# Optimization experiments

Hardware: AMD Instinct MI355X
Metric: run time of the kernel (lower is better)

## Reference

```python
import jax, jax.numpy as jnp
import numpy as np

B, T, C, H = 8, 2048, 1024, 64  # batch, seq_len(block_size), embedding_size, head_size


def setup_inputs() -> dict:
    key = jax.random.key(0)
    kx, kk, kq, kv = jax.random.split(key, 4)
    x = jax.random.normal(kx, (B, T, C), dtype=jnp.float32)
    # nn.Linear(C, H, bias=False) weights, stored as [in, out] for x @ W
    s = 1.0 / np.sqrt(C)
    Wk = jax.random.uniform(kk, (C, H), dtype=jnp.float32, minval=-s, maxval=s)
    Wq = jax.random.uniform(kq, (C, H), dtype=jnp.float32, minval=-s, maxval=s)
    Wv = jax.random.uniform(kv, (C, H), dtype=jnp.float32, minval=-s, maxval=s)
    return {"x": x, "Wk": Wk, "Wq": Wq, "Wv": Wv}


def reference(x, Wk, Wq, Wv):
    Bx, Tx, Cx = x.shape
    k = jnp.einsum('btc,ch->bth', x, Wk)
    q = jnp.einsum('btc,ch->bth', x, Wq)
    v = jnp.einsum('btc,ch->bth', x, Wv)
    # NOTE: original scales by embedding dim C ** -0.5, not head_size
    scores = jnp.einsum('bth,bsh->bts', q, k) * (Cx ** -0.5)  # [B,T,T]
    causal = jnp.tril(jnp.ones((Tx, Tx), dtype=bool))
    scores = jnp.where(causal, scores, -jnp.inf)
    attn = jax.nn.softmax(scores, axis=-1)
    # dropout is identity in eval/deterministic mode
    out = jnp.einsum('bts,bsh->bth', attn, v)  # [B,T,H]
    return out
```

## Files before the change

### kernel.cpp

```cpp
#include <hip/hip_runtime.h>
#include <hip/hip_bf16.h>
#include <math.h>


#define BT 16384
#define TSEQ 2048
#define XST 72

typedef __attribute__((ext_vector_type(8))) __bf16 bf16x8;
typedef __attribute__((ext_vector_type(8))) unsigned short ushort8;
typedef __attribute__((ext_vector_type(4))) float floatx4;

#define MFMA16(a, b, c) __builtin_amdgcn_mfma_f32_16x16x32_bf16( \
    __builtin_bit_cast(bf16x8, (a)), __builtin_bit_cast(bf16x8, (b)), (c), 0, 0, 0)

__device__ inline unsigned short f2bf(float f) {
  unsigned u = __builtin_bit_cast(unsigned, f);
  u += 0x7FFFu + ((u >> 16) & 1u);
  return (unsigned short)(u >> 16);
}
__device__ inline float bf2f(unsigned short s) {
  return __builtin_bit_cast(float, (unsigned)s << 16);
}
__device__ inline unsigned long long pack4bf(floatx4 f) {
  return (unsigned long long)f2bf(f[0]) | ((unsigned long long)f2bf(f[1]) << 16) |
         ((unsigned long long)f2bf(f[2]) << 32) | ((unsigned long long)f2bf(f[3]) << 48);
}
__device__ inline ushort8 pack8bf(floatx4 a, floatx4 b) {
  ushort8 t;
#pragma unroll
  for (int i = 0; i < 4; ++i) t[i] = f2bf(a[i]);
#pragma unroll
  for (int i = 0; i < 4; ++i) t[4 + i] = f2bf(b[i]);
  return t;
}
__device__ inline void glds16(const unsigned short* g, unsigned short* l) {
  __builtin_amdgcn_global_load_lds(
      (const __attribute__((address_space(1))) unsigned int*)g,
      (__attribute__((address_space(3))) unsigned int*)l, 16, 0, 0);
}

__global__ __launch_bounds__(256) void wt2_kernel(
    const float* __restrict__ Wq, const float* __restrict__ Wk,
    const float* __restrict__ Wv, unsigned short* __restrict__ Wt2) {
  __shared__ float ls[64][65];
  const int m = blockIdx.x >> 4;
  const int kci = blockIdx.x & 15;
  const int c0 = kci << 6;
  const float* __restrict__ W = (m == 0) ? Wq : (m == 1) ? Wk : Wv;
  const int tid = threadIdx.x;
#pragma unroll
  for (int i = 0; i < 16; ++i) {
    int idx = tid + (i << 8);
    int cl = idx >> 6, h = idx & 63;
    ls[cl][h] = W[(c0 + cl) * 64 + h];
  }
  __syncthreads();
  const int w = tid >> 6, lane = tid & 63;
  const int quad = lane >> 4, l16 = lane & 15;
  const int nt = (m << 2) + w;
#pragma unroll
  for (int half = 0; half < 2; ++half) {
    ushort8 t;
#pragma unroll
    for (int j = 0; j < 8; ++j)
      t[j] = f2bf(ls[(half << 5) + (quad << 3) + j][(w << 4) + l16]);
    *(ushort8*)(Wt2 + ((size_t)(((nt << 4) + kci) * 2 + half) << 9) +
                (lane << 3)) = t;
  }
}

#define BB0 9216
#define BBS 12288
#define XBS 4608

__global__ __launch_bounds__(512) void qkv_mfma(
    const float* __restrict__ x, const unsigned short* __restrict__ Wt2,
    unsigned short* __restrict__ Qf, unsigned short* __restrict__ Kf,
    unsigned short* __restrict__ Vf) {
  __shared__ unsigned short smem[33792];

  const int tid = threadIdx.x;
  const int w = tid >> 6, lane = tid & 63;
  const int quad = lane >> 4, l16 = lane & 15;
  const int wr = w >> 2, wn = w & 3;
  const int r0 = blockIdx.x << 6;

  const int xrow = (w << 3) + (lane >> 3);
  const int xcol = (lane & 7) << 3;
  const float* __restrict__ xp = x + (size_t)(r0 + xrow) * 1024 + xcol;
  const int xw_u16 = xrow * XST + xcol;

  floatx4 acc[2][3];
#pragma unroll
  for (int rt = 0; rt < 2; ++rt)
#pragma unroll
    for (int n = 0; n < 3; ++n) acc[rt][n] = (floatx4){0.f, 0.f, 0.f, 0.f};

  floatx4 pf[2][2];

#pragma unroll
  for (int i = 0; i < 3; ++i) {
    const int f = 3 * w + i;
    glds16(Wt2 + ((size_t)(((f >> 1) << 4) * 2 + (f & 1)) << 9) + (lane << 3),
           &smem[BB0 + (f << 9)]);
  }
  pf[0][0] = *(const floatx4*)(xp);
  pf[0][1] = *(const floatx4*)(xp + 4);
  pf[1][0] = *(const floatx4*)(xp + 64);
  pf[1][1] = *(const floatx4*)(xp + 68);
  *(ushort8*)&smem[xw_u16] = pack8bf(pf[0][0], pf[0][1]);
  asm volatile("s_waitcnt lgkmcnt(0)");
  __builtin_amdgcn_sched_barrier(0);
  __builtin_amdgcn_s_barrier();
  __builtin_amdgcn_sched_barrier(0);

#pragma unroll
  for (int c = 0; c < 16; ++c) {
    const int cur = c & 1, nxt = cur ^ 1;
    if (c + 1 < 16) {
#pragma unroll
      for (int i = 0; i < 3; ++i) {
        const int f = 3 * w + i;
        glds16(Wt2 + ((size_t)((((f >> 1) << 4) + (c + 1)) * 2 + (f & 1)) << 9) +
                   (lane << 3),
               &smem[BB0 + nxt * BBS + (f << 9)]);
      }
      *(ushort8*)&smem[nxt * XBS + xw_u16] =
          pack8bf(pf[(c + 1) & 1][0], pf[(c + 1) & 1][1]);
    }
    if (c + 2 < 16) {
      pf[c & 1][0] = *(const floatx4*)(xp + ((c + 2) << 6));
      pf[c & 1][1] = *(const floatx4*)(xp + ((c + 2) << 6) + 4);
    }
    __builtin_amdgcn_sched_barrier(0);

    ushort8 af[2][2];
#pragma unroll
    for (int rt = 0; rt < 2; ++rt)
#pragma unroll
      for (int h = 0; h < 2; ++h)
        af[rt][h] = *(const ushort8*)&smem[cur * XBS +
            ((wr << 5) + (rt << 4) + l16) * XST + (h << 5) + (quad << 3)];
    ushort8 bfr[3][2];
#pragma unroll
    for (int n = 0; n < 3; ++n)
#pragma unroll
      for (int h = 0; h < 2; ++h)
        bfr[n][h] = *(const ushort8*)&smem[BB0 + cur * BBS +
            ((((3 * wn + n) << 1) + h) << 9) + (lane << 3)];
#pragma unroll
    for (int h = 0; h < 2; ++h)
#pragma unroll
      for (int rt = 0; rt < 2; ++rt)
#pragma unroll
        for (int n = 0; n < 3; ++n)
          acc[rt][n] = MFMA16(af[rt][h], bfr[n][h], acc[rt][n]);

    __builtin_amdgcn_sched_barrier(0);
    if (c < 14) { asm volatile("s_waitcnt vmcnt(2)"); }
    else        { asm volatile("s_waitcnt vmcnt(0)"); }
    asm volatile("s_waitcnt lgkmcnt(0)");
    __builtin_amdgcn_sched_barrier(0);
    __builtin_amdgcn_s_barrier();
    __builtin_amdgcn_sched_barrier(0);
  }

#pragma unroll
  for (int n = 0; n < 3; ++n) {
    const int nt = 3 * wn + n;
    const int m = nt >> 2, hg = nt & 3;
#pragma unroll
    for (int rt = 0; rt < 2; ++rt) {
      const int rowb = (wr << 5) + (rt << 4) + (quad << 2);
      if (m < 2) {
#pragma unroll
        for (int r = 0; r < 4; ++r)
          smem[m * XBS + (rowb + r) * XST + (hg << 4) + l16] =
              f2bf(acc[rt][n][r]);
      } else {
        *(unsigned long long*)&smem[2 * XBS + ((hg << 4) + l16) * XST + rowb] =
            pack4bf(acc[rt][n]);
      }
    }
  }
  __syncthreads();

  const int b = blockIdx.x >> 5, st = blockIdx.x & 31;
#pragma unroll
  for (int i = 0; i < 3; ++i) {
    const int f = w * 3 + i;
    const int m = f >> 3, idx = f & 7, grp = idx >> 1, kh = idx & 1;
    ushort8 t = *(const ushort8*)&smem[m * XBS + ((grp << 4) + l16) * XST +
                                       (kh << 5) + (quad << 3)];
    unsigned short* dst;
    if (m == 0)
      dst = Qf + (((size_t)(b * 128 + (st << 2) + grp) * 2 + kh) << 9);
    else if (m == 1)
      dst = Kf + (((size_t)((b * 32 + st) * 4 + grp) * 2 + kh) << 9);
    else
      dst = Vf + (((size_t)((b * 32 + st) * 4 + grp) * 2 + kh) << 9);
    *(ushort8*)(dst + (lane << 3)) = t;
  }
}

__global__ __launch_bounds__(128) void attn_part(
    const unsigned short* __restrict__ Qf, const unsigned short* __restrict__ Kf,
    const unsigned short* __restrict__ Vf, float* __restrict__ part) {
  __shared__ unsigned short Pw[2][16 * XST];

  const int tid = threadIdx.x;
  const int w = tid >> 6, lane = tid & 63;
  const int quad = lane >> 4, l16 = lane & 15;
  const int b = blockIdx.x / 288;
  const int rem = blockIdx.x - b * 288;
  const int e = rem >> 1, half = rem & 1;
  int g = 0;
#pragma unroll
  for (int gg = 1; gg < 8; ++gg) g += (e >= 2 * gg * (gg + 1)) ? 1 : 0;
  const int rem2 = e - 2 * g * (g + 1);
  const int qt = (g << 2) + rem2 / (g + 1);
  const int ch = rem2 - (rem2 / (g + 1)) * (g + 1);
  const int s0 = ch << 2;
  const int s1 = min(s0 + 4, qt + 1);
  const int rg = (half << 1) + w;
  const int r16 = (qt << 2) + rg;

  const unsigned short* qbase =
      Qf + ((((size_t)b * 128 + r16) * 2) << 9) + (lane << 3);
  ushort8 qf0 = *(const ushort8*)qbase;
  ushort8 qf1 = *(const ushort8*)(qbase + 512);

  floatx4 acc[4], lacc;
#pragma unroll
  for (int nt = 0; nt < 4; ++nt) acc[nt] = (floatx4){0.f, 0.f, 0.f, 0.f};
  lacc = (floatx4){0.f, 0.f, 0.f, 0.f};
  const ushort8 ones = {0x3F80, 0x3F80, 0x3F80, 0x3F80,
                        0x3F80, 0x3F80, 0x3F80, 0x3F80};

#define KVIDX(ss, nt, kh) \
  (((((size_t)(b * 32 + (ss)) << 2) + (nt)) * 2 + (kh)) << 9)

  ushort8 bk[4][2];
#pragma unroll
  for (int nt = 0; nt < 4; ++nt)
#pragma unroll
    for (int kh = 0; kh < 2; ++kh)
      bk[nt][kh] = *(const ushort8*)(Kf + KVIDX(s0, nt, kh) + (lane << 3));

  for (int s = s0; s < s1; ++s) {
    const int sn = (s + 1 < s1) ? s + 1 : s;
    ushort8 bv[4][2];
#pragma unroll
    for (int nt = 0; nt < 4; ++nt)
#pragma unroll
      for (int kh = 0; kh < 2; ++kh)
        bv[nt][kh] = *(const ushort8*)(Vf + KVIDX(s, nt, kh) + (lane << 3));
    ushort8 bkn[4][2];
#pragma unroll
    for (int nt = 0; nt < 4; ++nt)
#pragma unroll
      for (int kh = 0; kh < 2; ++kh)
        bkn[nt][kh] = *(const ushort8*)(Kf + KVIDX(sn, nt, kh) + (lane << 3));

    floatx4 sf[4];
#pragma unroll
    for (int nt = 0; nt < 4; ++nt) {
      sf[nt] = (floatx4){0.f, 0.f, 0.f, 0.f};
      sf[nt] = MFMA16(qf0, bk[nt][0], sf[nt]);
      sf[nt] = MFMA16(qf1, bk[nt][1], sf[nt]);
    }

    const bool diag = (s == qt);
    const int qrow = (rg << 4) + (quad << 2);
#pragma unroll
    for (int nt = 0; nt < 4; ++nt) {
      const int keyl = (nt << 4) + l16;
#pragma unroll
      for (int r = 0; r < 4; ++r) {
        float ev = __expf(sf[nt][r] * 0.03125f);
        if (diag && keyl > ((qt << 6) - (qt << 6)) + qrow + r) ev = 0.f;
        Pw[w][((quad << 2) + r) * XST + keyl] = f2bf(ev);
      }
    }

#pragma unroll
    for (int kh = 0; kh < 2; ++kh) {
      ushort8 pa = *(const ushort8*)&Pw[w][l16 * XST + (kh << 5) + (quad << 3)];
      lacc = MFMA16(pa, ones, lacc);
#pragma unroll
      for (int nt = 0; nt < 4; ++nt) acc[nt] = MFMA16(pa, bv[nt][kh], acc[nt]);
    }
#pragma unroll
    for (int nt = 0; nt < 4; ++nt) {
      bk[nt][0] = bkn[nt][0];
      bk[nt][1] = bkn[nt][1];
    }
  }
#undef KVIDX

  float* slot = part + (size_t)(b * 144 + e) * 2112;
  if (l16 == 0) {
#pragma unroll
    for (int r = 0; r < 4; ++r) slot[(rg << 4) + (quad << 2) + r] = lacc[r];
  }
  unsigned short* op = (unsigned short*)(slot + 64);
#pragma unroll
  for (int nt = 0; nt < 4; ++nt)
#pragma unroll
    for (int r = 0; r < 4; ++r)
      op[((rg << 4) + (quad << 2) + r) * 64 + (nt << 4) + l16] = f2bf(acc[nt][r]);
}

__global__ __launch_bounds__(256) void attn_combine(
    const float* __restrict__ part, float* __restrict__ out) {
  const int rh = blockIdx.x & 1;
  const int bqt = blockIdx.x >> 1;
  const int b = bqt >> 5, qt = bqt & 31;
  const int tid = threadIdx.x;
  const int row = (rh << 5) + (tid >> 3);
  const int hseg = (tid & 7) << 3;
  const int g = qt >> 2;
  const int nch = g + 1;
  const int ebase = 2 * g * (g + 1) + (qt & 3) * (g + 1);

  float l = 0.f;
  float ov[8];
#pragma unroll
  for (int i = 0; i < 8; ++i) ov[i] = 0.f;
  for (int c = 0; c < nch; ++c) {
    const float* slot = part + (size_t)(b * 144 + ebase + c) * 2112;
    l += slot[row];
    ushort8 o0 = *(const ushort8*)((const unsigned short*)(slot + 64) +
                                   row * 64 + hseg);
#pragma unroll
    for (int i = 0; i < 8; ++i) ov[i] += bf2f(o0[i]);
  }
  const float inv = 1.f / l;
  float* o = out + ((size_t)(b * TSEQ + (qt << 6) + row)) * 64 + hseg;
#pragma unroll
  for (int i = 0; i < 8; ++i) o[i] = ov[i] * inv;
}

extern "C" void kernel_launch(void* const* d_in, const int* in_sizes, int n_in,
                              void* d_out, int out_size, void* d_ws, size_t ws_size,
                              hipStream_t stream) {
  const float* x  = (const float*)d_in[0];
  const float* Wk = (const float*)d_in[1];
  const float* Wq = (const float*)d_in[2];
  const float* Wv = (const float*)d_in[3];

  unsigned short* Qfw = (unsigned short*)d_ws;
  unsigned short* Kfw = Qfw + (size_t)BT * 64;
  unsigned short* Vfw = Kfw + (size_t)BT * 64;
  unsigned short* Wt2 = Vfw + (size_t)BT * 64;
  float* part = (float*)(Wt2 + 3 * 64 * 1024);

  wt2_kernel<<<48, 256, 0, stream>>>(Wq, Wk, Wv, Wt2);
  qkv_mfma<<<256, 512, 0, stream>>>(x, Wt2, Qfw, Kfw, Vfw);
  attn_part<<<2304, 128, 0, stream>>>(Qfw, Kfw, Vfw, part);
  attn_combine<<<512, 256, 0, stream>>>(part, (float*)d_out);
}
```

Measured before the change: 132.5 us.

## Fuse all four stages into one cooperative persistent kernel with grid syncs

Replaces the four separate launches (weight transpose, QKV projection, partial attention, combine) with a single cooperative kernel of 256 blocks that separates the phases with grid.sync. The attention phase becomes a persistent loop in which each wave handles work units. The QKV GEMM weight pipeline also moves from double to triple buffering with a deeper prefetch. The aim is to remove launch gaps and kernel boundaries, at the cost of grid-wide barriers and less parallelism in the attention phase (256 blocks instead of 2304).

```diff
diff --git a/kernel.cpp b/kernel.cpp
--- a/kernel.cpp
+++ b/kernel.cpp
@@ -1,6 +1,9 @@
 #include <hip/hip_runtime.h>
 #include <hip/hip_bf16.h>
+#include <hip/hip_cooperative_groups.h>
 #include <math.h>
+
+namespace cg = cooperative_groups;
 
 
 #define BT 16384
@@ -40,306 +43,320 @@
       (__attribute__((address_space(3))) unsigned int*)l, 16, 0, 0);
 }
 
-__global__ __launch_bounds__(256) void wt2_kernel(
-    const float* __restrict__ Wq, const float* __restrict__ Wk,
-    const float* __restrict__ Wv, unsigned short* __restrict__ Wt2) {
-  __shared__ float ls[64][65];
-  const int m = blockIdx.x >> 4;
-  const int kci = blockIdx.x & 15;
-  const int c0 = kci << 6;
-  const float* __restrict__ W = (m == 0) ? Wq : (m == 1) ? Wk : Wv;
-  const int tid = threadIdx.x;
-#pragma unroll
-  for (int i = 0; i < 16; ++i) {
-    int idx = tid + (i << 8);
-    int cl = idx >> 6, h = idx & 63;
-    ls[cl][h] = W[(c0 + cl) * 64 + h];
-  }
-  __syncthreads();
-  const int w = tid >> 6, lane = tid & 63;
-  const int quad = lane >> 4, l16 = lane & 15;
-  const int nt = (m << 2) + w;
-#pragma unroll
-  for (int half = 0; half < 2; ++half) {
-    ushort8 t;
-#pragma unroll
-    for (int j = 0; j < 8; ++j)
-      t[j] = f2bf(ls[(half << 5) + (quad << 3) + j][(w << 4) + l16]);
-    *(ushort8*)(Wt2 + ((size_t)(((nt << 4) + kci) * 2 + half) << 9) +
-                (lane << 3)) = t;
-  }
-}
-
+#define XBS 4608
 #define BB0 9216
 #define BBS 12288
-#define XBS 4608
-
-__global__ __launch_bounds__(512) void qkv_mfma(
-    const float* __restrict__ x, const unsigned short* __restrict__ Wt2,
-    unsigned short* __restrict__ Qf, unsigned short* __restrict__ Kf,
-    unsigned short* __restrict__ Vf) {
-  __shared__ unsigned short smem[33792];
-
+
+__global__ __launch_bounds__(512, 2) void fused_attn(
+    const float* __restrict__ x, const float* __restrict__ Wq,
+    const float* __restrict__ Wk, const float* __restrict__ Wv,
+    unsigned short* __restrict__ Wt2, unsigned short* __restrict__ Qf,
+    unsigned short* __restrict__ Kf, unsigned short* __restrict__ Vf,
+    float* __restrict__ part, float* __restrict__ out) {
+  __shared__ __align__(16) unsigned short smem[46080];
   const int tid = threadIdx.x;
   const int w = tid >> 6, lane = tid & 63;
   const int quad = lane >> 4, l16 = lane & 15;
-  const int wr = w >> 2, wn = w & 3;
-  const int r0 = blockIdx.x << 6;
-
-  const int xrow = (w << 3) + (lane >> 3);
-  const int xcol = (lane & 7) << 3;
-  const float* __restrict__ xp = x + (size_t)(r0 + xrow) * 1024 + xcol;
-  const int xw_u16 = xrow * XST + xcol;
-
-  floatx4 acc[2][3];
-#pragma unroll
-  for (int rt = 0; rt < 2; ++rt)
-#pragma unroll
-    for (int n = 0; n < 3; ++n) acc[rt][n] = (floatx4){0.f, 0.f, 0.f, 0.f};
-
-  floatx4 pf[2][2];
-
-#pragma unroll
-  for (int i = 0; i < 3; ++i) {
-    const int f = 3 * w + i;
-    glds16(Wt2 + ((size_t)(((f >> 1) << 4) * 2 + (f & 1)) << 9) + (lane << 3),
-           &smem[BB0 + (f << 9)]);
+  cg::grid_group grid = cg::this_grid();
+
+  if (blockIdx.x < 48) {
+    float* ls = (float*)smem;
+    const int m = blockIdx.x >> 4, kci = blockIdx.x & 15, c0 = kci << 6;
+    const float* __restrict__ W = (m == 0) ? Wq : (m == 1) ? Wk : Wv;
+#pragma unroll
+    for (int i = 0; i < 8; ++i) {
+      int idx = tid + (i << 9);
+      int cl = idx >> 6, h = idx & 63;
+      ls[cl * 65 + h] = W[(c0 + cl) * 64 + h];
+    }
+    __syncthreads();
+    if (tid < 256) {
+      const int nt = (m << 2) + w;
+#pragma unroll
+      for (int half = 0; half < 2; ++half) {
+        ushort8 t;
+#pragma unroll
+        for (int j = 0; j < 8; ++j)
+          t[j] = f2bf(ls[((half << 5) + (quad << 3) + j) * 65 + (w << 4) + l16]);
+        *(ushort8*)(Wt2 + ((size_t)(((nt << 4) + kci) * 2 + half) << 9) +
+                    (lane << 3)) = t;
+      }
+    }
   }
-  pf[0][0] = *(const floatx4*)(xp);
-  pf[0][1] = *(const floatx4*)(xp + 4);
-  pf[1][0] = *(const floatx4*)(xp + 64);
-  pf[1][1] = *(const floatx4*)(xp + 68);
-  *(ushort8*)&smem[xw_u16] = pack8bf(pf[0][0], pf[0][1]);
-  asm volatile("s_waitcnt lgkmcnt(0)");
-  __builtin_amdgcn_sched_barrier(0);
-  __builtin_amdgcn_s_barrier();
-  __builtin_amdgcn_sched_barrier(0);
-
-#pragma unroll
-  for (int c = 0; c < 16; ++c) {
-    const int cur = c & 1, nxt = cur ^ 1;
-    if (c + 1 < 16) {
-#pragma unroll
-      for (int i = 0; i < 3; ++i) {
-        const int f = 3 * w + i;
-        glds16(Wt2 + ((size_t)((((f >> 1) << 4) + (c + 1)) * 2 + (f & 1)) << 9) +
-                   (lane << 3),
-               &smem[BB0 + nxt * BBS + (f << 9)]);
-      }
-      *(ushort8*)&smem[nxt * XBS + xw_u16] =
-          pack8bf(pf[(c + 1) & 1][0], pf[(c + 1) & 1][1]);
-    }
-    if (c + 2 < 16) {
-      pf[c & 1][0] = *(const floatx4*)(xp + ((c + 2) << 6));
-      pf[c & 1][1] = *(const floatx4*)(xp + ((c + 2) << 6) + 4);
-    }
-    __builtin_amdgcn_sched_barrier(0);
-
-    ushort8 af[2][2];
+  __threadfence();
+  grid.sync();
+
+  {
+    const int wr = w >> 2, wn = w & 3;
+    const int r0 = blockIdx.x << 6;
+    const int xrow = (w << 3) + (lane >> 3);
+    const int xcol = (lane & 7) << 3;
+    const float* __restrict__ xp = x + (size_t)(r0 + xrow) * 1024 + xcol;
+    const int xw_u16 = xrow * XST + xcol;
+
+    floatx4 acc[2][3];
 #pragma unroll
     for (int rt = 0; rt < 2; ++rt)
 #pragma unroll
+      for (int n = 0; n < 3; ++n) acc[rt][n] = (floatx4){0.f, 0.f, 0.f, 0.f};
+
+    floatx4 pf[2][2];
+    pf[0][0] = *(const floatx4*)(xp);
+    pf[0][1] = *(const floatx4*)(xp + 4);
+    __builtin_amdgcn_sched_barrier(0);
+#pragma unroll
+    for (int i = 0; i < 3; ++i) {
+      const int f = 3 * w + i;
+      glds16(Wt2 + ((size_t)(((f >> 1) << 4) * 2 + (f & 1)) << 9) + (lane << 3),
+             &smem[BB0 + (f << 9)]);
+    }
+    __builtin_amdgcn_sched_barrier(0);
+    pf[1][0] = *(const floatx4*)(xp + 64);
+    pf[1][1] = *(const floatx4*)(xp + 68);
+    __builtin_amdgcn_sched_barrier(0);
+#pragma unroll
+    for (int i = 0; i < 3; ++i) {
+      const int f = 3 * w + i;
+      glds16(Wt2 + ((size_t)((((f >> 1) << 4) + 1) * 2 + (f & 1)) << 9) +
+                 (lane << 3),
+             &smem[BB0 + BBS + (f << 9)]);
+    }
+    __builtin_amdgcn_sched_barrier(0);
+    *(ushort8*)&smem[xw_u16] = pack8bf(pf[0][0], pf[0][1]);
+    __builtin_amdgcn_sched_barrier(0);
+    asm volatile("s_waitcnt vmcnt(5)");
+    asm volatile("s_waitcnt lgkmcnt(0)");
+    __builtin_amdgcn_sched_barrier(0);
+    __builtin_amdgcn_s_barrier();
+    __builtin_amdgcn_sched_barrier(0);
+
+#pragma unroll
+    for (int c = 0; c < 16; ++c) {
+      if (c + 1 < 16)
+        *(ushort8*)&smem[((c + 1) & 1) * XBS + xw_u16] =
+            pack8bf(pf[(c + 1) & 1][0], pf[(c + 1) & 1][1]);
+      __builtin_amdgcn_sched_barrier(0);
+      if (c + 2 < 16) {
+        pf[c & 1][0] = *(const floatx4*)(xp + ((c + 2) << 6));
+        pf[c & 1][1] = *(const floatx4*)(xp + ((c + 2) << 6) + 4);
+        __builtin_amdgcn_sched_barrier(0);
+#pragma unroll
+        for (int i = 0; i < 3; ++i) {
+          const int f = 3 * w + i;
+          glds16(Wt2 + ((size_t)((((f >> 1) << 4) + (c + 2)) * 2 + (f & 1)) << 9) +
+                     (lane << 3),
+                 &smem[BB0 + ((c + 2) % 3) * BBS + (f << 9)]);
+        }
+      }
+      __builtin_amdgcn_sched_barrier(0);
+
+      ushort8 af[2][2];
+#pragma unroll
+      for (int rt = 0; rt < 2; ++rt)
+#pragma unroll
+        for (int h = 0; h < 2; ++h)
+          af[rt][h] = *(const ushort8*)&smem[(c & 1) * XBS +
+              ((wr << 5) + (rt << 4) + l16) * XST + (h << 5) + (quad << 3)];
+      ushort8 bfr[3][2];
+#pragma unroll
+      for (int n = 0; n < 3; ++n)
+#pragma unroll
+        for (int h = 0; h < 2; ++h)
+          bfr[n][h] = *(const ushort8*)&smem[BB0 + (c % 3) * BBS +
+              ((((3 * wn + n) << 1) + h) << 9) + (lane << 3)];
+#pragma unroll
       for (int h = 0; h < 2; ++h)
-        af[rt][h] = *(const ushort8*)&smem[cur * XBS +
-            ((wr << 5) + (rt << 4) + l16) * XST + (h << 5) + (quad << 3)];
-    ushort8 bfr[3][2];
-#pragma unroll
-    for (int n = 0; n < 3; ++n)
-#pragma unroll
-      for (int h = 0; h < 2; ++h)
-        bfr[n][h] = *(const ushort8*)&smem[BB0 + cur * BBS +
-            ((((3 * wn + n) << 1) + h) << 9) + (lane << 3)];
-#pragma unroll
-    for (int h = 0; h < 2; ++h)
-#pragma unroll
-      for (int rt = 0; rt < 2; ++rt)
-#pragma unroll
-        for (int n = 0; n < 3; ++n)
-          acc[rt][n] = MFMA16(af[rt][h], bfr[n][h], acc[rt][n]);
-
-    __builtin_amdgcn_sched_barrier(0);
-    if (c < 14) { asm volatile("s_waitcnt vmcnt(2)"); }
-    else        { asm volatile("s_waitcnt vmcnt(0)"); }
-    asm volatile("s_waitcnt lgkmcnt(0)");
-    __builtin_amdgcn_sched_barrier(0);
-    __builtin_amdgcn_s_barrier();
-    __builtin_amdgcn_sched_barrier(0);
+#pragma unroll
+        for (int rt = 0; rt < 2; ++rt)
+#pragma unroll
+          for (int n = 0; n < 3; ++n)
+            acc[rt][n] = MFMA16(af[rt][h], bfr[n][h], acc[rt][n]);
+
+      __builtin_amdgcn_sched_barrier(0);
+      if (c < 14) { asm volatile("s_waitcnt vmcnt(5)"); }
+      else        { asm volatile("s_waitcnt vmcnt(0)"); }
+      asm volatile("s_waitcnt lgkmcnt(0)");
+      __builtin_amdgcn_sched_barrier(0);
+      __builtin_amdgcn_s_barrier();
+      __builtin_amdgcn_sched_barrier(0);
+    }
+
+#pragma unroll
+    for (int n = 0; n < 3; ++n) {
+      const int nt = 3 * wn + n;
+      const int m = nt >> 2, hg = nt & 3;
+#pragma unroll
+      for (int rt = 0; rt < 2; ++rt) {
+        const int rowb = (wr << 5) + (rt << 4) + (quad << 2);
+        if (m < 2) {
+#pragma unroll
+          for (int r = 0; r < 4; ++r)
+            smem[m * XBS + (rowb + r) * XST + (hg << 4) + l16] =
+                f2bf(acc[rt][n][r]);
+        } else {
+          *(unsigned long long*)&smem[2 * XBS + ((hg << 4) + l16) * XST + rowb] =
+              pack4bf(acc[rt][n]);
+        }
+      }
+    }
+    __syncthreads();
+
+    const int bb = blockIdx.x >> 5, st = blockIdx.x & 31;
+#pragma unroll
+    for (int i = 0; i < 3; ++i) {
+      const int f = w * 3 + i;
+      const int m = f >> 3, idx = f & 7, grp = idx >> 1, kh = idx & 1;
+      ushort8 t = *(const ushort8*)&smem[m * XBS + ((grp << 4) + l16) * XST +
+                                         (kh << 5) + (quad << 3)];
+      unsigned short* dst;
+      if (m == 0)
+        dst = Qf + (((size_t)(bb * 128 + (st << 2) + grp) * 2 + kh) << 9);
+      else if (m == 1)
+        dst = Kf + (((size_t)((bb * 32 + st) * 4 + grp) * 2 + kh) << 9);
+      else
+        dst = Vf + (((size_t)((bb * 32 + st) * 4 + grp) * 2 + kh) << 9);
+      *(ushort8*)(dst + (lane << 3)) = t;
+    }
   }
-
-#pragma unroll
-  for (int n = 0; n < 3; ++n) {
-    const int nt = 3 * wn + n;
-    const int m = nt >> 2, hg = nt & 3;
-#pragma unroll
-    for (int rt = 0; rt < 2; ++rt) {
-      const int rowb = (wr << 5) + (rt << 4) + (quad << 2);
-      if (m < 2) {
-#pragma unroll
-        for (int r = 0; r < 4; ++r)
-          smem[m * XBS + (rowb + r) * XST + (hg << 4) + l16] =
-              f2bf(acc[rt][n][r]);
-      } else {
-        *(unsigned long long*)&smem[2 * XBS + ((hg << 4) + l16) * XST + rowb] =
-            pack4bf(acc[rt][n]);
-      }
-    }
-  }
-  __syncthreads();
-
-  const int b = blockIdx.x >> 5, st = blockIdx.x & 31;
-#pragma unroll
-  for (int i = 0; i < 3; ++i) {
-    const int f = w * 3 + i;
-    const int m = f >> 3, idx = f & 7, grp = idx >> 1, kh = idx & 1;
-    ushort8 t = *(const ushort8*)&smem[m * XBS + ((grp << 4) + l16) * XST +
-                                       (kh << 5) + (quad << 3)];
-    unsigned short* dst;
-    if (m == 0)
-      dst = Qf + (((size_t)(b * 128 + (st << 2) + grp) * 2 + kh) << 9);
-    else if (m == 1)
-      dst = Kf + (((size_t)((b * 32 + st) * 4 + grp) * 2 + kh) << 9);
-    else
-      dst = Vf + (((size_t)((b * 32 + st) * 4 + grp) * 2 + kh) << 9);
-    *(ushort8*)(dst + (lane << 3)) = t;
-  }
-}
-
-__global__ __launch_bounds__(128) void attn_part(
-    const unsigned short* __restrict__ Qf, const unsigned short* __restrict__ Kf,
-    const unsigned short* __restrict__ Vf, float* __restrict__ part) {
-  __shared__ unsigned short Pw[2][16 * XST];
-
-  const int tid = threadIdx.x;
-  const int w = tid >> 6, lane = tid & 63;
-  const int quad = lane >> 4, l16 = lane & 15;
-  const int b = blockIdx.x / 288;
-  const int rem = blockIdx.x - b * 288;
-  const int e = rem >> 1, half = rem & 1;
-  int g = 0;
-#pragma unroll
-  for (int gg = 1; gg < 8; ++gg) g += (e >= 2 * gg * (gg + 1)) ? 1 : 0;
-  const int rem2 = e - 2 * g * (g + 1);
-  const int qt = (g << 2) + rem2 / (g + 1);
-  const int ch = rem2 - (rem2 / (g + 1)) * (g + 1);
-  const int s0 = ch << 2;
-  const int s1 = min(s0 + 4, qt + 1);
-  const int rg = (half << 1) + w;
-  const int r16 = (qt << 2) + rg;
-
-  const unsigned short* qbase =
-      Qf + ((((size_t)b * 128 + r16) * 2) << 9) + (lane << 3);
-  ushort8 qf0 = *(const ushort8*)qbase;
-  ushort8 qf1 = *(const ushort8*)(qbase + 512);
-
-  floatx4 acc[4], lacc;
-#pragma unroll
-  for (int nt = 0; nt < 4; ++nt) acc[nt] = (floatx4){0.f, 0.f, 0.f, 0.f};
-  lacc = (floatx4){0.f, 0.f, 0.f, 0.f};
-  const ushort8 ones = {0x3F80, 0x3F80, 0x3F80, 0x3F80,
-                        0x3F80, 0x3F80, 0x3F80, 0x3F80};
+  __threadfence();
+  grid.sync();
+
+  {
+    unsigned short* Pww = &smem[w * 1152];
+    const ushort8 ones = {0x3F80, 0x3F80, 0x3F80, 0x3F80,
+                          0x3F80, 0x3F80, 0x3F80, 0x3F80};
+    for (int u = (blockIdx.x << 3) + w; u < 4608; u += 2048) {
+      const int b = u / 576;
+      const int ru = u - b * 576;
+      const int e = ru >> 2;
+      const int rg = ru & 3;
+      int g = 0;
+#pragma unroll
+      for (int gg = 1; gg < 8; ++gg) g += (e >= 2 * gg * (gg + 1)) ? 1 : 0;
+      const int rem2 = e - 2 * g * (g + 1);
+      const int qt = (g << 2) + rem2 / (g + 1);
+      const int ch = rem2 - (rem2 / (g + 1)) * (g + 1);
+      const int s0 = ch << 2;
+      const int s1 = (s0 + 4 < qt + 1) ? s0 + 4 : qt + 1;
+      const int r16 = (qt << 2) + rg;
+
+      const unsigned short* qbase =
+          Qf + ((((size_t)b * 128 + r16) * 2) << 9) + (lane << 3);
+      ushort8 qf0 = *(const ushort8*)qbase;
+      ushort8 qf1 = *(const ushort8*)(qbase + 512);
+
+      floatx4 acc[4], lacc;
+#pragma unroll
+      for (int nt = 0; nt < 4; ++nt) acc[nt] = (floatx4){0.f, 0.f, 0.f, 0.f};
+      lacc = (floatx4){0.f, 0.f, 0.f, 0.f};
 
 #define KVIDX(ss, nt, kh) \
   (((((size_t)(b * 32 + (ss)) << 2) + (nt)) * 2 + (kh)) << 9)
 
-  ushort8 bk[4][2];
-#pragma unroll
-  for (int nt = 0; nt < 4; ++nt)
-#pragma unroll
-    for (int kh = 0; kh < 2; ++kh)
-      bk[nt][kh] = *(const ushort8*)(Kf + KVIDX(s0, nt, kh) + (lane << 3));
-
-  for (int s = s0; s < s1; ++s) {
-    const int sn = (s + 1 < s1) ? s + 1 : s;
-    ushort8 bv[4][2];
-#pragma unroll
-    for (int nt = 0; nt < 4; ++nt)
-#pragma unroll
-      for (int kh = 0; kh < 2; ++kh)
-        bv[nt][kh] = *(const ushort8*)(Vf + KVIDX(s, nt, kh) + (lane << 3));
-    ushort8 bkn[4][2];
-#pragma unroll
-    for (int nt = 0; nt < 4; ++nt)
-#pragma unroll
-      for (int kh = 0; kh < 2; ++kh)
-        bkn[nt][kh] = *(const ushort8*)(Kf + KVIDX(sn, nt, kh) + (lane << 3));
-
-    floatx4 sf[4];
-#pragma unroll
-    for (int nt = 0; nt < 4; ++nt) {
-      sf[nt] = (floatx4){0.f, 0.f, 0.f, 0.f};
-      sf[nt] = MFMA16(qf0, bk[nt][0], sf[nt]);
-      sf[nt] = MFMA16(qf1, bk[nt][1], sf[nt]);
-    }
-
-    const bool diag = (s == qt);
-    const int qrow = (rg << 4) + (quad << 2);
-#pragma unroll
-    for (int nt = 0; nt < 4; ++nt) {
-      const int keyl = (nt << 4) + l16;
-#pragma unroll
-      for (int r = 0; r < 4; ++r) {
-        float ev = __expf(sf[nt][r] * 0.03125f);
-        if (diag && keyl > ((qt << 6) - (qt << 6)) + qrow + r) ev = 0.f;
-        Pw[w][((quad << 2) + r) * XST + keyl] = f2bf(ev);
-      }
-    }
-
-#pragma unroll
-    for (int kh = 0; kh < 2; ++kh) {
-      ushort8 pa = *(const ushort8*)&Pw[w][l16 * XST + (kh << 5) + (quad << 3)];
-      lacc = MFMA16(pa, ones, lacc);
-#pragma unroll
-      for (int nt = 0; nt < 4; ++nt) acc[nt] = MFMA16(pa, bv[nt][kh], acc[nt]);
-    }
-#pragma unroll
-    for (int nt = 0; nt < 4; ++nt) {
-      bk[nt][0] = bkn[nt][0];
-      bk[nt][1] = bkn[nt][1];
+      ushort8 bk[4][2];
+#pragma unroll
+      for (int nt = 0; nt < 4; ++nt)
+#pragma unroll
+        for (int kh = 0; kh < 2; ++kh)
+          bk[nt][kh] = *(const ushort8*)(Kf + KVIDX(s0, nt, kh) + (lane << 3));
+
+      for (int s = s0; s < s1; ++s) {
+        const int sn = (s + 1 < s1) ? s + 1 : s;
+        ushort8 bv[4][2];
+#pragma unroll
+        for (int nt = 0; nt < 4; ++nt)
+#pragma unroll
+          for (int kh = 0; kh < 2; ++kh)
+            bv[nt][kh] = *(const ushort8*)(Vf + KVIDX(s, nt, kh) + (lane << 3));
+        ushort8 bkn[4][2];
+#pragma unroll
+        for (int nt = 0; nt < 4; ++nt)
+#pragma unroll
+          for (int kh = 0; kh < 2; ++kh)
+            bkn[nt][kh] = *(const ushort8*)(Kf + KVIDX(sn, nt, kh) + (lane << 3));
+
+        floatx4 sf[4];
+#pragma unroll
+        for (int nt = 0; nt < 4; ++nt) {
+          sf[nt] = (floatx4){0.f, 0.f, 0.f, 0.f};
+          sf[nt] = MFMA16(qf0, bk[nt][0], sf[nt]);
+          sf[nt] = MFMA16(qf1, bk[nt][1], sf[nt]);
+        }
+
+        const bool diag = (s == qt);
+        const int qrow = (rg << 4) + (quad << 2);
+#pragma unroll
+        for (int nt = 0; nt < 4; ++nt) {
+          const int keyl = (nt << 4) + l16;
+#pragma unroll
+          for (int r = 0; r < 4; ++r) {
+            float ev = __expf(sf[nt][r] * 0.03125f);
+            if (diag && keyl > qrow + r) ev = 0.f;
+            Pww[((quad << 2) + r) * XST + keyl] = f2bf(ev);
+          }
+        }
+
+#pragma unroll
+        for (int kh = 0; kh < 2; ++kh) {
+          ushort8 pa = *(const ushort8*)&Pww[l16 * XST + (kh << 5) + (quad << 3)];
+          lacc = MFMA16(pa, ones, lacc);
+#pragma unroll
+          for (int nt = 0; nt < 4; ++nt) acc[nt] = MFMA16(pa, bv[nt][kh], acc[nt]);
+        }
+#pragma unroll
+        for (int nt = 0; nt < 4; ++nt) {
+          bk[nt][0] = bkn[nt][0];
+          bk[nt][1] = bkn[nt][1];
+        }
+      }
+#undef KVIDX
+
+      float* slot = part + (size_t)(b * 144 + e) * 2112;
+      if (l16 == 0) {
+#pragma unroll
+        for (int r = 0; r < 4; ++r) slot[(rg << 4) + (quad << 2) + r] = lacc[r];
+      }
+      unsigned short* op = (unsigned short*)(slot + 64);
+#pragma unroll
+      for (int nt = 0; nt < 4; ++nt)
+#pragma unroll
+        for (int r = 0; r < 4; ++r)
+          op[((rg << 4) + (quad << 2) + r) * 64 + (nt << 4) + l16] =
+              f2bf(acc[nt][r]);
     }
   }
-#undef KVIDX
-
-  float* slot = part + (size_t)(b * 144 + e) * 2112;
-  if (l16 == 0) {
-#pragma unroll
-    for (int r = 0; r < 4; ++r) slot[(rg << 4) + (quad << 2) + r] = lacc[r];
+  __threadfence();
+  grid.sync();
+
+  {
+    const int ob = (blockIdx.x << 1) | (tid >> 8);
+    const int t = tid & 255;
+    const int rh = ob & 1;
+    const int bqt = ob >> 1;
+    const int b = bqt >> 5, qt = bqt & 31;
+    const int row = (rh << 5) + (t >> 3);
+    const int hseg = (t & 7) << 3;
+    const int g = qt >> 2;
+    const int nch = g + 1;
+    const int ebase = 2 * g * (g + 1) + (qt & 3) * (g + 1);
+
+    float l = 0.f;
+    float ov[8];
+#pragma unroll
+    for (int i = 0; i < 8; ++i) ov[i] = 0.f;
+    for (int c = 0; c < nch; ++c) {
+      const float* slot = part + (size_t)(b * 144 + ebase + c) * 2112;
+      l += slot[row];
+      ushort8 o0 = *(const ushort8*)((const unsigned short*)(slot + 64) +
+                                     row * 64 + hseg);
+#pragma unroll
+      for (int i = 0; i < 8; ++i) ov[i] += bf2f(o0[i]);
+    }
+    const float inv = 1.f / l;
+    float* o = out + ((size_t)(b * TSEQ + (qt << 6) + row)) * 64 + hseg;
+#pragma unroll
+    for (int i = 0; i < 8; ++i) o[i] = ov[i] * inv;
   }
-  unsigned short* op = (unsigned short*)(slot + 64);
-#pragma unroll
-  for (int nt = 0; nt < 4; ++nt)
-#pragma unroll
-    for (int r = 0; r < 4; ++r)
-      op[((rg << 4) + (quad << 2) + r) * 64 + (nt << 4) + l16] = f2bf(acc[nt][r]);
-}
-
-__global__ __launch_bounds__(256) void attn_combine(
-    const float* __restrict__ part, float* __restrict__ out) {
-  const int rh = blockIdx.x & 1;
-  const int bqt = blockIdx.x >> 1;
-  const int b = bqt >> 5, qt = bqt & 31;
-  const int tid = threadIdx.x;
-  const int row = (rh << 5) + (tid >> 3);
-  const int hseg = (tid & 7) << 3;
-  const int g = qt >> 2;
-  const int nch = g + 1;
-  const int ebase = 2 * g * (g + 1) + (qt & 3) * (g + 1);
-
-  float l = 0.f;
-  float ov[8];
-#pragma unroll
-  for (int i = 0; i < 8; ++i) ov[i] = 0.f;
-  for (int c = 0; c < nch; ++c) {
-    const float* slot = part + (size_t)(b * 144 + ebase + c) * 2112;
-    l += slot[row];
-    ushort8 o0 = *(const ushort8*)((const unsigned short*)(slot + 64) +
-                                   row * 64 + hseg);
-#pragma unroll
-    for (int i = 0; i < 8; ++i) ov[i] += bf2f(o0[i]);
-  }
-  const float inv = 1.f / l;
-  float* o = out + ((size_t)(b * TSEQ + (qt << 6) + row)) * 64 + hseg;
-#pragma unroll
-  for (int i = 0; i < 8; ++i) o[i] = ov[i] * inv;
 }
 
 extern "C" void kernel_launch(void* const* d_in, const int* in_sizes, int n_in,
@@ -355,9 +372,11 @@
   unsigned short* Vfw = Kfw + (size_t)BT * 64;
   unsigned short* Wt2 = Vfw + (size_t)BT * 64;
   float* part = (float*)(Wt2 + 3 * 64 * 1024);
-
-  wt2_kernel<<<48, 256, 0, stream>>>(Wq, Wk, Wv, Wt2);
-  qkv_mfma<<<256, 512, 0, stream>>>(x, Wt2, Qfw, Kfw, Vfw);
-  attn_part<<<2304, 128, 0, stream>>>(Qfw, Kfw, Vfw, part);
-  attn_combine<<<512, 256, 0, stream>>>(part, (float*)d_out);
-}
+  float* outp = (float*)d_out;
+
+  void* args[] = {(void*)&x,   (void*)&Wq,  (void*)&Wk,  (void*)&Wv,
+                  (void*)&Wt2, (void*)&Qfw, (void*)&Kfw, (void*)&Vfw,
+                  (void*)&part, (void*)&outp};
+  hipLaunchCooperativeKernel((void*)fused_attn, dim3(256), dim3(512), args, 0,
+                             stream);
+}
```

Result: slower. 400.7 us (+202.4%).

## Triple-buffer QKV weight loads and stage shared K/V tiles in LDS for attention

Applied to the files above, without the earlier changes.

In the QKV projection, weight tiles now use a three-slot LDS ring and are prefetched two chunks ahead instead of one, with the vmcnt waits adjusted to match. The attention partial kernel now runs 4 waves per block covering all 64 query rows of a tile. K/V tiles are loaded once per block into double-buffered LDS with direct global-to-LDS loads and shared across the waves, where before each wave read them straight from global memory. The intent is to deepen memory latency hiding and cut redundant K/V global traffic, at the cost of more LDS per block, extra barriers, and half as many blocks in the attention launch.

```diff
diff --git a/kernel.cpp b/kernel.cpp
--- a/kernel.cpp
+++ b/kernel.cpp
@@ -70,22 +70,21 @@
   }
 }
 
+#define XBS 4608
 #define BB0 9216
 #define BBS 12288
-#define XBS 4608
 
 __global__ __launch_bounds__(512) void qkv_mfma(
     const float* __restrict__ x, const unsigned short* __restrict__ Wt2,
     unsigned short* __restrict__ Qf, unsigned short* __restrict__ Kf,
     unsigned short* __restrict__ Vf) {
-  __shared__ unsigned short smem[33792];
+  __shared__ __align__(16) unsigned short smem[46080];
 
   const int tid = threadIdx.x;
   const int w = tid >> 6, lane = tid & 63;
   const int quad = lane >> 4, l16 = lane & 15;
   const int wr = w >> 2, wn = w & 3;
   const int r0 = blockIdx.x << 6;
-
   const int xrow = (w << 3) + (lane >> 3);
   const int xcol = (lane & 7) << 3;
   const float* __restrict__ xp = x + (size_t)(r0 + xrow) * 1024 + xcol;
@@ -98,18 +97,30 @@
     for (int n = 0; n < 3; ++n) acc[rt][n] = (floatx4){0.f, 0.f, 0.f, 0.f};
 
   floatx4 pf[2][2];
-
+  pf[0][0] = *(const floatx4*)(xp);
+  pf[0][1] = *(const floatx4*)(xp + 4);
+  __builtin_amdgcn_sched_barrier(0);
 #pragma unroll
   for (int i = 0; i < 3; ++i) {
     const int f = 3 * w + i;
     glds16(Wt2 + ((size_t)(((f >> 1) << 4) * 2 + (f & 1)) << 9) + (lane << 3),
            &smem[BB0 + (f << 9)]);
   }
-  pf[0][0] = *(const floatx4*)(xp);
-  pf[0][1] = *(const floatx4*)(xp + 4);
+  __builtin_amdgcn_sched_barrier(0);
   pf[1][0] = *(const floatx4*)(xp + 64);
   pf[1][1] = *(const floatx4*)(xp + 68);
+  __builtin_amdgcn_sched_barrier(0);
+#pragma unroll
+  for (int i = 0; i < 3; ++i) {
+    const int f = 3 * w + i;
+    glds16(Wt2 + ((size_t)((((f >> 1) << 4) + 1) * 2 + (f & 1)) << 9) +
+               (lane << 3),
+           &smem[BB0 + BBS + (f << 9)]);
+  }
+  __builtin_amdgcn_sched_barrier(0);
   *(ushort8*)&smem[xw_u16] = pack8bf(pf[0][0], pf[0][1]);
+  __builtin_amdgcn_sched_barrier(0);
+  asm volatile("s_waitcnt vmcnt(5)");
   asm volatile("s_waitcnt lgkmcnt(0)");
   __builtin_amdgcn_sched_barrier(0);
   __builtin_amdgcn_s_barrier();
@@ -117,21 +128,21 @@
 
 #pragma unroll
   for (int c = 0; c < 16; ++c) {
-    const int cur = c & 1, nxt = cur ^ 1;
-    if (c + 1 < 16) {
-#pragma unroll
-      for (int i = 0; i < 3; ++i) {
-        const int f = 3 * w + i;
-        glds16(Wt2 + ((size_t)((((f >> 1) << 4) + (c + 1)) * 2 + (f & 1)) << 9) +
-                   (lane << 3),
-               &smem[BB0 + nxt * BBS + (f << 9)]);
-      }
-      *(ushort8*)&smem[nxt * XBS + xw_u16] =
+    if (c + 1 < 16)
+      *(ushort8*)&smem[((c + 1) & 1) * XBS + xw_u16] =
           pack8bf(pf[(c + 1) & 1][0], pf[(c + 1) & 1][1]);
-    }
+    __builtin_amdgcn_sched_barrier(0);
     if (c + 2 < 16) {
       pf[c & 1][0] = *(const floatx4*)(xp + ((c + 2) << 6));
       pf[c & 1][1] = *(const floatx4*)(xp + ((c + 2) << 6) + 4);
+      __builtin_amdgcn_sched_barrier(0);
+#pragma unroll
+      for (int i = 0; i < 3; ++i) {
+        const int f = 3 * w + i;
+        glds16(Wt2 + ((size_t)((((f >> 1) << 4) + (c + 2)) * 2 + (f & 1)) << 9) +
+                   (lane << 3),
+               &smem[BB0 + ((c + 2) % 3) * BBS + (f << 9)]);
+      }
     }
     __builtin_amdgcn_sched_barrier(0);
 
@@ -140,14 +151,14 @@
     for (int rt = 0; rt < 2; ++rt)
 #pragma unroll
       for (int h = 0; h < 2; ++h)
-        af[rt][h] = *(const ushort8*)&smem[cur * XBS +
+        af[rt][h] = *(const ushort8*)&smem[(c & 1) * XBS +
             ((wr << 5) + (rt << 4) + l16) * XST + (h << 5) + (quad << 3)];
     ushort8 bfr[3][2];
 #pragma unroll
     for (int n = 0; n < 3; ++n)
 #pragma unroll
       for (int h = 0; h < 2; ++h)
-        bfr[n][h] = *(const ushort8*)&smem[BB0 + cur * BBS +
+        bfr[n][h] = *(const ushort8*)&smem[BB0 + (c % 3) * BBS +
             ((((3 * wn + n) << 1) + h) << 9) + (lane << 3)];
 #pragma unroll
     for (int h = 0; h < 2; ++h)
@@ -158,7 +169,7 @@
           acc[rt][n] = MFMA16(af[rt][h], bfr[n][h], acc[rt][n]);
 
     __builtin_amdgcn_sched_barrier(0);
-    if (c < 14) { asm volatile("s_waitcnt vmcnt(2)"); }
+    if (c < 14) { asm volatile("s_waitcnt vmcnt(5)"); }
     else        { asm volatile("s_waitcnt vmcnt(0)"); }
     asm volatile("s_waitcnt lgkmcnt(0)");
     __builtin_amdgcn_sched_barrier(0);
@@ -204,17 +215,17 @@
   }
 }
 
-__global__ __launch_bounds__(128) void attn_part(
+__global__ __launch_bounds__(256, 3) void attn_part(
     const unsigned short* __restrict__ Qf, const unsigned short* __restrict__ Kf,
     const unsigned short* __restrict__ Vf, float* __restrict__ part) {
-  __shared__ unsigned short Pw[2][16 * XST];
+  __shared__ __align__(16) unsigned short KV[2][8192];
+  __shared__ unsigned short Pw[4][16 * XST];
 
   const int tid = threadIdx.x;
   const int w = tid >> 6, lane = tid & 63;
   const int quad = lane >> 4, l16 = lane & 15;
-  const int b = blockIdx.x / 288;
-  const int rem = blockIdx.x - b * 288;
-  const int e = rem >> 1, half = rem & 1;
+  const int b = blockIdx.x / 144;
+  const int e = blockIdx.x - b * 144;
   int g = 0;
 #pragma unroll
   for (int gg = 1; gg < 8; ++gg) g += (e >= 2 * gg * (gg + 1)) ? 1 : 0;
@@ -222,14 +233,36 @@
   const int qt = (g << 2) + rem2 / (g + 1);
   const int ch = rem2 - (rem2 / (g + 1)) * (g + 1);
   const int s0 = ch << 2;
-  const int s1 = min(s0 + 4, qt + 1);
-  const int rg = (half << 1) + w;
-  const int r16 = (qt << 2) + rg;
+  const int s1 = (s0 + 4 < qt + 1) ? s0 + 4 : qt + 1;
+  const int r16 = (qt << 2) + w;
+
+#define KVIDX(ss, nt, kh) \
+  (((((size_t)(b * 32 + (ss)) << 2) + (nt)) * 2 + (kh)) << 9)
+#define STAGE_KV(ss, db)                                                     \
+  {                                                                          \
+    _Pragma("unroll") for (int r_ = 0; r_ < 4; ++r_) {                       \
+      const int f_ = (r_ << 2) + w;                                          \
+      const unsigned short* src_ =                                           \
+          (f_ < 8) ? Kf + KVIDX(ss, (f_ >> 1), (f_ & 1)) + (lane << 3)       \
+                   : Vf + KVIDX(ss, (f_ >> 1) - 4, (f_ & 1)) + (lane << 3);  \
+      glds16(src_, &KV[db][f_ << 9]);                                        \
+    }                                                                        \
+  }
 
   const unsigned short* qbase =
       Qf + ((((size_t)b * 128 + r16) * 2) << 9) + (lane << 3);
   ushort8 qf0 = *(const ushort8*)qbase;
   ushort8 qf1 = *(const ushort8*)(qbase + 512);
+  __builtin_amdgcn_sched_barrier(0);
+
+  STAGE_KV(s0, 0);
+  __builtin_amdgcn_sched_barrier(0);
+  STAGE_KV((s0 + 1 < s1) ? s0 + 1 : s1 - 1, 1);
+  __builtin_amdgcn_sched_barrier(0);
+  asm volatile("s_waitcnt vmcnt(4)");
+  __builtin_amdgcn_sched_barrier(0);
+  __builtin_amdgcn_s_barrier();
+  __builtin_amdgcn_sched_barrier(0);
 
   floatx4 acc[4], lacc;
 #pragma unroll
@@ -238,30 +271,25 @@
   const ushort8 ones = {0x3F80, 0x3F80, 0x3F80, 0x3F80,
                         0x3F80, 0x3F80, 0x3F80, 0x3F80};
 
-#define KVIDX(ss, nt, kh) \
-  (((((size_t)(b * 32 + (ss)) << 2) + (nt)) * 2 + (kh)) << 9)
-
-  ushort8 bk[4][2];
-#pragma unroll
-  for (int nt = 0; nt < 4; ++nt)
-#pragma unroll
-    for (int kh = 0; kh < 2; ++kh)
-      bk[nt][kh] = *(const ushort8*)(Kf + KVIDX(s0, nt, kh) + (lane << 3));
-
   for (int s = s0; s < s1; ++s) {
-    const int sn = (s + 1 < s1) ? s + 1 : s;
-    ushort8 bv[4][2];
+    const int cur = (s - s0) & 1;
+    ushort8 bk[4][2], bv[4][2];
 #pragma unroll
     for (int nt = 0; nt < 4; ++nt)
 #pragma unroll
-      for (int kh = 0; kh < 2; ++kh)
-        bv[nt][kh] = *(const ushort8*)(Vf + KVIDX(s, nt, kh) + (lane << 3));
-    ushort8 bkn[4][2];
-#pragma unroll
-    for (int nt = 0; nt < 4; ++nt)
-#pragma unroll
-      for (int kh = 0; kh < 2; ++kh)
-        bkn[nt][kh] = *(const ushort8*)(Kf + KVIDX(sn, nt, kh) + (lane << 3));
+      for (int kh = 0; kh < 2; ++kh) {
+        bk[nt][kh] = *(const ushort8*)&KV[cur][((((nt << 1) + kh)) << 9) +
+                                              (lane << 3)];
+        bv[nt][kh] = *(const ushort8*)&KV[cur][(((8 + (nt << 1) + kh)) << 9) +
+                                              (lane << 3)];
+      }
+    asm volatile("s_waitcnt lgkmcnt(0)");
+    __builtin_amdgcn_sched_barrier(0);
+    __builtin_amdgcn_s_barrier();
+    __builtin_amdgcn_sched_barrier(0);
+
+    STAGE_KV((s + 2 < s1) ? s + 2 : s1 - 1, cur);
+    __builtin_amdgcn_sched_barrier(0);
 
     floatx4 sf[4];
 #pragma unroll
@@ -272,14 +300,14 @@
     }
 
     const bool diag = (s == qt);
-    const int qrow = (rg << 4) + (quad << 2);
+    const int qrow = (w << 4) + (quad << 2);
 #pragma unroll
     for (int nt = 0; nt < 4; ++nt) {
       const int keyl = (nt << 4) + l16;
 #pragma unroll
       for (int r = 0; r < 4; ++r) {
         float ev = __expf(sf[nt][r] * 0.03125f);
-        if (diag && keyl > ((qt << 6) - (qt << 6)) + qrow + r) ev = 0.f;
+        if (diag && keyl > qrow + r) ev = 0.f;
         Pw[w][((quad << 2) + r) * XST + keyl] = f2bf(ev);
       }
     }
@@ -291,25 +319,27 @@
 #pragma unroll
       for (int nt = 0; nt < 4; ++nt) acc[nt] = MFMA16(pa, bv[nt][kh], acc[nt]);
     }
-#pragma unroll
-    for (int nt = 0; nt < 4; ++nt) {
-      bk[nt][0] = bkn[nt][0];
-      bk[nt][1] = bkn[nt][1];
-    }
-  }
+
+    __builtin_amdgcn_sched_barrier(0);
+    asm volatile("s_waitcnt vmcnt(4)");
+    __builtin_amdgcn_sched_barrier(0);
+    __builtin_amdgcn_s_barrier();
+    __builtin_amdgcn_sched_barrier(0);
+  }
+#undef STAGE_KV
 #undef KVIDX
 
   float* slot = part + (size_t)(b * 144 + e) * 2112;
   if (l16 == 0) {
 #pragma unroll
-    for (int r = 0; r < 4; ++r) slot[(rg << 4) + (quad << 2) + r] = lacc[r];
+    for (int r = 0; r < 4; ++r) slot[(w << 4) + (quad << 2) + r] = lacc[r];
   }
   unsigned short* op = (unsigned short*)(slot + 64);
 #pragma unroll
   for (int nt = 0; nt < 4; ++nt)
 #pragma unroll
     for (int r = 0; r < 4; ++r)
-      op[((rg << 4) + (quad << 2) + r) * 64 + (nt << 4) + l16] = f2bf(acc[nt][r]);
+      op[((w << 4) + (quad << 2) + r) * 64 + (nt << 4) + l16] = f2bf(acc[nt][r]);
 }
 
 __global__ __launch_bounds__(256) void attn_combine(
@@ -358,6 +388,6 @@
 
   wt2_kernel<<<48, 256, 0, stream>>>(Wq, Wk, Wv, Wt2);
   qkv_mfma<<<256, 512, 0, stream>>>(x, Wt2, Qfw, Kfw, Vfw);
-  attn_part<<<2304, 128, 0, stream>>>(Qfw, Kfw, Vfw, part);
+  attn_part<<<1152, 256, 0, stream>>>(Qfw, Kfw, Vfw, part);
   attn_combine<<<512, 256, 0, stream>>>(part, (float*)d_out);
 }
```

New measurement: 130.7 us. Within noise of the previous version (-1.4%).
